# Optimization experiments

Hardware: AMD Instinct MI355X
Metric: run time of the kernel (lower is better)

The kernel has to match this reference:

```python
import jax, jax.numpy as jnp
import numpy as np

LN_EPS = 1e-5

def layer_norm(x, g, b):
    mu = jnp.mean(x, axis=-1, keepdims=True)
    var = jnp.var(x, axis=-1, keepdims=True)
    return (x - mu) * jax.lax.rsqrt(var + LN_EPS) * g + b

def setup_inputs() -> dict:
    key = jax.random.key(0)
    ks = jax.random.split(key, 4)
    d = 2048
    bs, win_len, obj_num = 8, 64, 36
    return {
        "visual_feats": jax.random.normal(ks[0], (bs, win_len, d), dtype=jnp.float32),
        "obj_feats": jax.random.normal(ks[1], (bs, win_len, obj_num, d), dtype=jnp.float32),
        "W_v": jax.random.normal(ks[2], (d, d), dtype=jnp.float32) * (1.0 / np.sqrt(d)),
        "b_v": jnp.zeros((d,), dtype=jnp.float32),
        "W_o": jax.random.normal(ks[3], (d, d), dtype=jnp.float32) * (1.0 / np.sqrt(d)),
        "b_o": jnp.zeros((d,), dtype=jnp.float32),
        "ln_v_g": jnp.ones((d,), dtype=jnp.float32),
        "ln_v_b": jnp.zeros((d,), dtype=jnp.float32),
        "ln_o_g": jnp.ones((d,), dtype=jnp.float32),
        "ln_o_b": jnp.zeros((d,), dtype=jnp.float32),
        "ln_ov_g": jnp.ones((d,), dtype=jnp.float32),
        "ln_ov_b": jnp.zeros((d,), dtype=jnp.float32),
    }

def reference(visual_feats, obj_feats, W_v, b_v, W_o, b_o,
              ln_v_g, ln_v_b, ln_o_g, ln_o_b, ln_ov_g, ln_ov_b):
    bs, win_len, obj_num, obj_size = obj_feats.shape
    # visual branch: linear -> tanh -> LN   [bs, F, d]
    ve = layer_norm(jnp.tanh(visual_feats @ W_v + b_v), ln_v_g, ln_v_b)
    # object branch: linear -> flatten frames*objects -> tanh -> LN  [bs, N, d]
    oe = (obj_feats @ W_o + b_o).reshape(bs, win_len * obj_num, obj_size)
    oe = layer_norm(jnp.tanh(oe), ln_o_g, ln_o_b)
    # adjacency: [bs, N, F], softmax over N (object axis, dim=1)
    adj = jnp.einsum('bnd,bfd->bnf', oe, ve) / jnp.sqrt(jnp.asarray(obj_size, dtype=oe.dtype))
    adj = jax.nn.softmax(adj, axis=1)
    # aggregate objects per frame: (oe^T @ adj)^T -> [bs, F, d]
    obj_agg = jnp.einsum('bnd,bnf->bfd', oe, adj)
    return layer_norm(jnp.tanh(obj_agg + ve), ln_ov_g, ln_ov_b)
```

## Files before the change

### kernel.cpp

```cpp
#include <hip/hip_runtime.h>
#include <cstdint>
#include <cstddef>


typedef __attribute__((ext_vector_type(4))) float f32x4;
typedef __attribute__((ext_vector_type(4))) unsigned int u32x4;
typedef __attribute__((ext_vector_type(8))) short bf16x8;

#define DD 2048
#define BS 8
#define FF 64
#define NOBJ 2304
#define MO 18432
#define MV 512

__device__ __forceinline__ unsigned short f2bf(float f) {
  unsigned int u = __float_as_uint(f);
  u += 0x7fffu + ((u >> 16) & 1u);
  return (unsigned short)(u >> 16);
}
__device__ __forceinline__ unsigned int pk2(float a, float b) {
  return (unsigned int)f2bf(a) | ((unsigned int)f2bf(b) << 16);
}
__device__ __forceinline__ float bf2f(unsigned short u) {
  return __uint_as_float((unsigned int)u << 16);
}

typedef __attribute__((address_space(1))) const unsigned int gas_u32;
typedef __attribute__((address_space(3))) unsigned int las_u32;
__device__ __forceinline__ void gl_lds16(const void* g, void* l) {
  __builtin_amdgcn_global_load_lds((gas_u32*)g, (las_u32*)l, 16, 0, 0);
}

__global__ __launch_bounds__(256) void k_cvt_bf16(const float* __restrict__ X,
                                                  unsigned short* __restrict__ O,
                                                  int n16) {
  int idx = blockIdx.x * 256 + threadIdx.x;
  const int stride = gridDim.x * 256;
  for (int i = idx; i < n16; i += stride) {
    const f32x4* src = (const f32x4*)(X + (size_t)i * 16);
    f32x4 a = src[0], b = src[1], c = src[2], d = src[3];
    u32x4 p = {pk2(a.x, a.y), pk2(a.z, a.w), pk2(b.x, b.y), pk2(b.z, b.w)};
    u32x4 q = {pk2(c.x, c.y), pk2(c.z, c.w), pk2(d.x, d.y), pk2(d.z, d.w)};
    u32x4* dst = (u32x4*)(O + (size_t)i * 16);
    dst[0] = p;
    dst[1] = q;
  }
}

__global__ __launch_bounds__(256) void k_wprep2(const float* __restrict__ Wv,
                                                const float* __restrict__ Wo,
                                                unsigned short* __restrict__ WvT,
                                                unsigned short* __restrict__ WoT) {
  __shared__ unsigned short sh[64][65];
  const float* W = blockIdx.z ? Wo : Wv;
  unsigned short* Wt = blockIdx.z ? WoT : WvT;
  const int t = threadIdx.x;
  const int kb = blockIdx.x * 64, nb = blockIdx.y * 64;
  {
    const int rk = t >> 2, seg = t & 3;
    const float* src = W + (size_t)(kb + rk) * DD + nb + seg * 16;
#pragma unroll
    for (int q = 0; q < 4; ++q) {
      f32x4 x = *(const f32x4*)(src + q * 4);
      sh[rk][seg * 16 + q * 4 + 0] = f2bf(x.x);
      sh[rk][seg * 16 + q * 4 + 1] = f2bf(x.y);
      sh[rk][seg * 16 + q * 4 + 2] = f2bf(x.z);
      sh[rk][seg * 16 + q * 4 + 3] = f2bf(x.w);
    }
  }
  __syncthreads();
  {
    const int nn = t >> 2, ks = t & 3;
    unsigned int o[8];
#pragma unroll
    for (int j = 0; j < 8; ++j)
      o[j] = (unsigned int)sh[ks * 16 + 2 * j][nn] |
             ((unsigned int)sh[ks * 16 + 2 * j + 1][nn] << 16);
    u32x4 p0 = {o[0], o[1], o[2], o[3]};
    u32x4 p1 = {o[4], o[5], o[6], o[7]};
    unsigned short* dst = Wt + (size_t)(nb + nn) * DD + kb + ks * 16;
    ((u32x4*)dst)[0] = p0;
    ((u32x4*)dst)[1] = p1;
  }
}

__global__ __launch_bounds__(512, 1) void k_gemm_bbf(const unsigned short* __restrict__ A,
                                                     const unsigned short* __restrict__ Bt,
                                                     const float* __restrict__ bias,
                                                     unsigned short* __restrict__ T,
                                                     float* __restrict__ part) {
  __shared__ __align__(16) unsigned short lds[2 * 32768];
  const int tid = threadIdx.x;
  const int lane = tid & 63, wave = tid >> 6;
  const int r = lane & 15, g = lane >> 4;
  const int wm = wave >> 2, wn = wave & 3;

  const int orig = blockIdx.y * 8 + blockIdx.x;
  const int lin = (orig & 7) * 72 + (orig >> 3);
  const int bm = (lin >> 3) * 256;
  const int bn = (lin & 7) * 256;

  const int srow = tid >> 3;
  const int k16s = (tid & 7) ^ (srow & 7);
  const unsigned short* aS = A + (size_t)(bm + srow) * DD + k16s * 8;
  const unsigned short* bS = Bt + (size_t)(bn + srow) * DD + k16s * 8;

  auto stage = [&](int buf, int kt) {
    unsigned short* ab = lds + buf * 32768;
    unsigned short* bb = ab + 16384;
    const size_t ko = (size_t)kt * 64;
#pragma unroll
    for (int i = 0; i < 4; ++i)
      gl_lds16(aS + ko + (size_t)(i * 64) * DD, ab + ((i * 512 + tid) << 3));
#pragma unroll
    for (int i = 0; i < 4; ++i)
      gl_lds16(bS + ko + (size_t)(i * 64) * DD, bb + ((i * 512 + tid) << 3));
  };

  const int rs = r & 7;
  const int s0 = ((0 + g) ^ rs) * 8;
  const int s1 = ((4 + g) ^ rs) * 8;
  const int abase = (wm * 128 + r) * 64;
  const int bbase = 16384 + (wn * 64 + r) * 64;

  f32x4 acc[8][4] = {};

  stage(0, 0);
  asm volatile("s_waitcnt vmcnt(0)" ::: "memory");
  __builtin_amdgcn_s_barrier();

  for (int kt = 0; kt < DD / 64; ++kt) {
    const unsigned short* bufp = lds + (kt & 1) * 32768;
    const bool st = (kt + 1 < DD / 64);
    if (st) stage((kt + 1) & 1, kt + 1);

    bf16x8 bAll[4][2];
#pragma unroll
    for (int ni = 0; ni < 4; ++ni) {
      const int ro = bbase + ni * 1024;
      bAll[ni][0] = *(const bf16x8*)(bufp + ro + s0);
      bAll[ni][1] = *(const bf16x8*)(bufp + ro + s1);
    }
#pragma unroll
    for (int q = 0; q < 4; ++q) {
      bf16x8 af[2][2];
#pragma unroll
      for (int mi = 0; mi < 2; ++mi) {
        const int ro = abase + (q * 32 + mi * 16) * 64;
        af[mi][0] = *(const bf16x8*)(bufp + ro + s0);
        af[mi][1] = *(const bf16x8*)(bufp + ro + s1);
      }
      __builtin_amdgcn_s_setprio(1);
#pragma unroll
      for (int mi = 0; mi < 2; ++mi)
#pragma unroll
        for (int ni = 0; ni < 4; ++ni) {
          acc[q * 2 + mi][ni] = __builtin_amdgcn_mfma_f32_16x16x32_bf16(
              af[mi][0], bAll[ni][0], acc[q * 2 + mi][ni], 0, 0, 0);
          acc[q * 2 + mi][ni] = __builtin_amdgcn_mfma_f32_16x16x32_bf16(
              af[mi][1], bAll[ni][1], acc[q * 2 + mi][ni], 0, 0, 0);
        }
      __builtin_amdgcn_s_setprio(0);
    }
    if (st) asm volatile("s_waitcnt vmcnt(0)" ::: "memory");
    __builtin_amdgcn_s_barrier();
  }

  float bv[4];
#pragma unroll
  for (int ni = 0; ni < 4; ++ni) bv[ni] = bias[bn + wn * 64 + ni * 16 + r];
  const int slot = ((lin & 7) << 2) + wn;
#pragma unroll
  for (int mi = 0; mi < 8; ++mi) {
#pragma unroll
    for (int i2 = 0; i2 < 4; ++i2) {
      const int row = bm + wm * 128 + mi * 16 + g * 4 + i2;
      unsigned short* trow = T + (size_t)row * DD + bn + wn * 64 + r;
      float s1 = 0.f, s2 = 0.f;
#pragma unroll
      for (int ni = 0; ni < 4; ++ni) {
        const float tv = tanhf(acc[mi][ni][i2] + bv[ni]);
        trow[ni * 16] = f2bf(tv);
        s1 += tv;
        s2 += tv * tv;
      }
#pragma unroll
      for (int m = 1; m < 16; m <<= 1) {
        s1 += __shfl_xor(s1, m, 64);
        s2 += __shfl_xor(s2, m, 64);
      }
      if (r == 0) {
        float2 p2 = make_float2(s1, s2);
        *(float2*)(part + (size_t)row * 64 + slot * 2) = p2;
      }
    }
  }
}

__global__ __launch_bounds__(256) void k_ep_ln2(const unsigned short* __restrict__ T,
                                                const float* __restrict__ part,
                                                const float* __restrict__ gw,
                                                const float* __restrict__ bw,
                                                unsigned short* __restrict__ obf) {
  const int row = blockIdx.x, t = threadIdx.x;
  float s1 = 0.f, s2 = 0.f;
  if (t < 32) {
    float2 p = ((const float2*)(part + (size_t)row * 64))[t];
    s1 = p.x;
    s2 = p.y;
  }
#pragma unroll
  for (int m = 1; m < 64; m <<= 1) {
    s1 += __shfl_xor(s1, m, 64);
    s2 += __shfl_xor(s2, m, 64);
  }
  __shared__ float sh[2];
  if (t == 0) {
    sh[0] = s1;
    sh[1] = s2;
  }
  __syncthreads();
  const float mean = sh[0] * (1.0f / DD);
  const float var = sh[1] * (1.0f / DD) - mean * mean;
  const float rstd = rsqrtf(var + 1e-5f);
  const size_t base = (size_t)row * DD + t * 8;
  u32x4 tin = *(const u32x4*)(T + base);
  f32x4 g0 = ((const f32x4*)(gw + t * 8))[0], g1 = ((const f32x4*)(gw + t * 8))[1];
  f32x4 bb0 = ((const f32x4*)(bw + t * 8))[0], bb1 = ((const f32x4*)(bw + t * 8))[1];
  float gv[8], bvv[8];
  gv[0] = g0.x; gv[1] = g0.y; gv[2] = g0.z; gv[3] = g0.w;
  gv[4] = g1.x; gv[5] = g1.y; gv[6] = g1.z; gv[7] = g1.w;
  bvv[0] = bb0.x; bvv[1] = bb0.y; bvv[2] = bb0.z; bvv[3] = bb0.w;
  bvv[4] = bb1.x; bvv[5] = bb1.y; bvv[6] = bb1.z; bvv[7] = bb1.w;
  float o[8];
#pragma unroll
  for (int j = 0; j < 4; ++j) {
    const float tl = bf2f((unsigned short)(tin[j] & 0xffffu));
    const float th = bf2f((unsigned short)(tin[j] >> 16));
    o[2 * j] = (tl - mean) * rstd * gv[2 * j] + bvv[2 * j];
    o[2 * j + 1] = (th - mean) * rstd * gv[2 * j + 1] + bvv[2 * j + 1];
  }
  u32x4 p = {pk2(o[0], o[1]), pk2(o[2], o[3]), pk2(o[4], o[5]), pk2(o[6], o[7])};
  *((u32x4*)(obf + base)) = p;
}

__global__ __launch_bounds__(256) void k_gemm_xw(const float* __restrict__ X,
                                                 const unsigned short* __restrict__ Wt,
                                                 const float* __restrict__ bias,
                                                 float* __restrict__ Y) {
  __shared__ __align__(16) unsigned short As[128 * 32];
  __shared__ __align__(16) unsigned short Bs[128 * 32];
  const int t = threadIdx.x;
  const int lane = t & 63, wave = t >> 6;
  const int r = lane & 15, g = lane >> 4;
  const int wm = wave >> 1, wn = wave & 1;
  const int bm = blockIdx.y * 128, bn = blockIdx.x * 128;
  const int arow = t >> 1, ah = t & 1;
  f32x4 acc[4][4] = {};
  const float* aptr = X + (size_t)(bm + arow) * DD + ah * 16;
  const unsigned short* bptr = Wt + (size_t)(bn + arow) * DD + ah * 16;
  for (int kt = 0; kt < DD / 32; ++kt) {
    const int kb = kt * 32;
    f32x4 a0 = *(const f32x4*)(aptr + kb);
    f32x4 a1 = *(const f32x4*)(aptr + kb + 4);
    f32x4 a2 = *(const f32x4*)(aptr + kb + 8);
    f32x4 a3 = *(const f32x4*)(aptr + kb + 12);
    u32x4 b0 = *(const u32x4*)(bptr + kb);
    u32x4 b1 = *(const u32x4*)(bptr + kb + 8);
    __syncthreads();
    u32x4 p0 = {pk2(a0.x, a0.y), pk2(a0.z, a0.w), pk2(a1.x, a1.y), pk2(a1.z, a1.w)};
    u32x4 p1 = {pk2(a2.x, a2.y), pk2(a2.z, a2.w), pk2(a3.x, a3.y), pk2(a3.z, a3.w)};
    ((u32x4*)As)[arow * 4 + ah * 2 + 0] = p0;
    ((u32x4*)As)[arow * 4 + ah * 2 + 1] = p1;
    ((u32x4*)Bs)[arow * 4 + ah * 2 + 0] = b0;
    ((u32x4*)Bs)[arow * 4 + ah * 2 + 1] = b1;
    __syncthreads();
    bf16x8 af[4], bfr[4];
#pragma unroll
    for (int m = 0; m < 4; ++m) af[m] = ((const bf16x8*)As)[(wm * 64 + m * 16 + r) * 4 + g];
#pragma unroll
    for (int n = 0; n < 4; ++n) bfr[n] = ((const bf16x8*)Bs)[(wn * 64 + n * 16 + r) * 4 + g];
#pragma unroll
    for (int m = 0; m < 4; ++m)
#pragma unroll
      for (int n = 0; n < 4; ++n)
        acc[m][n] = __builtin_amdgcn_mfma_f32_16x16x32_bf16(af[m], bfr[n], acc[m][n], 0, 0, 0);
  }
#pragma unroll
  for (int m = 0; m < 4; ++m) {
    const int row0 = bm + wm * 64 + m * 16 + g * 4;
#pragma unroll
    for (int n = 0; n < 4; ++n) {
      const int col = bn + wn * 64 + n * 16 + r;
      const float bvx = bias[col];
#pragma unroll
      for (int i = 0; i < 4; ++i)
        Y[(size_t)(row0 + i) * DD + col] = acc[m][n][i] + bvx;
    }
  }
}

__global__ __launch_bounds__(256) void k_ep_ln(const float* __restrict__ Y,
                                               const float* __restrict__ Y2,
                                               const float* __restrict__ gw,
                                               const float* __restrict__ bw,
                                               unsigned short* __restrict__ obf,
                                               float* __restrict__ of32) {
  const int row = blockIdx.x, t = threadIdx.x;
  const size_t base = (size_t)row * DD + t * 8;
  f32x4 v0 = ((const f32x4*)(Y + base))[0];
  f32x4 v1 = ((const f32x4*)(Y + base))[1];
  if (Y2 != nullptr) {
    v0 += ((const f32x4*)(Y2 + base))[0];
    v1 += ((const f32x4*)(Y2 + base))[1];
  }
  float tv[8];
#pragma unroll
  for (int j = 0; j < 4; ++j) {
    tv[j] = tanhf(v0[j]);
    tv[4 + j] = tanhf(v1[j]);
  }
  float s1 = 0.f, s2 = 0.f;
#pragma unroll
  for (int j = 0; j < 8; ++j) {
    s1 += tv[j];
    s2 += tv[j] * tv[j];
  }
#pragma unroll
  for (int m = 1; m < 64; m <<= 1) {
    s1 += __shfl_xor(s1, m, 64);
    s2 += __shfl_xor(s2, m, 64);
  }
  __shared__ float r1[4], r2[4];
  const int wave = t >> 6;
  if ((t & 63) == 0) {
    r1[wave] = s1;
    r2[wave] = s2;
  }
  __syncthreads();
  const float S1 = r1[0] + r1[1] + r1[2] + r1[3];
  const float S2 = r2[0] + r2[1] + r2[2] + r2[3];
  const float mean = S1 * (1.0f / DD);
  const float var = S2 * (1.0f / DD) - mean * mean;
  const float rstd = rsqrtf(var + 1e-5f);
  f32x4 g0 = ((const f32x4*)(gw + t * 8))[0], g1 = ((const f32x4*)(gw + t * 8))[1];
  f32x4 bb0 = ((const f32x4*)(bw + t * 8))[0], bb1 = ((const f32x4*)(bw + t * 8))[1];
  float o[8];
#pragma unroll
  for (int j = 0; j < 4; ++j) {
    o[j] = (tv[j] - mean) * rstd * g0[j] + bb0[j];
    o[4 + j] = (tv[4 + j] - mean) * rstd * g1[j] + bb1[j];
  }
  if (obf != nullptr) {
    u32x4 p = {pk2(o[0], o[1]), pk2(o[2], o[3]), pk2(o[4], o[5]), pk2(o[6], o[7])};
    *((u32x4*)(obf + base)) = p;
  }
  if (of32 != nullptr) {
    f32x4 w0 = {o[0], o[1], o[2], o[3]}, w1 = {o[4], o[5], o[6], o[7]};
    ((f32x4*)(of32 + base))[0] = w0;
    ((f32x4*)(of32 + base))[1] = w1;
  }
}

__global__ __launch_bounds__(256) void k_troe(const unsigned short* __restrict__ oe,
                                              unsigned short* __restrict__ oeT) {
  __shared__ unsigned short sh[64][65];
  const int t = threadIdx.x;
  const int b = blockIdx.z, nt = blockIdx.x, dt = blockIdx.y;
  {
    const int nn = t >> 2, seg = t & 3;
    const unsigned short* src = oe + ((size_t)b * NOBJ + nt * 64 + nn) * DD + dt * 64 + seg * 16;
    u32x4 x0 = ((const u32x4*)src)[0];
    u32x4 x1 = ((const u32x4*)src)[1];
    const unsigned short* px0 = (const unsigned short*)&x0;
    const unsigned short* px1 = (const unsigned short*)&x1;
#pragma unroll
    for (int j = 0; j < 8; ++j) {
      sh[nn][seg * 16 + j] = px0[j];
      sh[nn][seg * 16 + 8 + j] = px1[j];
    }
  }
  __syncthreads();
  {
    const int dd = t >> 2, ns = t & 3;
    unsigned int o[8];
#pragma unroll
    for (int j = 0; j < 8; ++j)
      o[j] = (unsigned int)sh[ns * 16 + 2 * j][dd] |
             ((unsigned int)sh[ns * 16 + 2 * j + 1][dd] << 16);
    u32x4 p0 = {o[0], o[1], o[2], o[3]};
    u32x4 p1 = {o[4], o[5], o[6], o[7]};
    unsigned short* dst = oeT + ((size_t)b * DD + dt * 64 + dd) * NOBJ + nt * 64 + ns * 16;
    ((u32x4*)dst)[0] = p0;
    ((u32x4*)dst)[1] = p1;
  }
}

__global__ __launch_bounds__(256) void k_gemm_adj(const unsigned short* __restrict__ oe,
                                                  const unsigned short* __restrict__ veb,
                                                  float* __restrict__ adjT) {
  __shared__ __align__(16) unsigned short As[128 * 32];
  __shared__ __align__(16) unsigned short Bs[64 * 32];
  const int t = threadIdx.x;
  const int lane = t & 63, wave = t >> 6;
  const int r = lane & 15, g = lane >> 4;
  const int wm = wave >> 1, wn = wave & 1;
  const int b = blockIdx.y, bm = blockIdx.x * 128;
  const int arow = t >> 1, ah = t & 1;
  const int br_ = t >> 2, bseg = t & 3;
  f32x4 acc[4][2] = {};
  const unsigned short* aptr = oe + ((size_t)b * NOBJ + bm + arow) * DD + ah * 16;
  const unsigned short* bptr = veb + ((size_t)b * FF + br_) * DD + bseg * 8;
  for (int kt = 0; kt < DD / 32; ++kt) {
    const int kb = kt * 32;
    u32x4 a0 = ((const u32x4*)(aptr + kb))[0];
    u32x4 a1 = ((const u32x4*)(aptr + kb))[1];
    u32x4 bvx = *(const u32x4*)(bptr + kb);
    __syncthreads();
    ((u32x4*)As)[arow * 4 + ah * 2 + 0] = a0;
    ((u32x4*)As)[arow * 4 + ah * 2 + 1] = a1;
    ((u32x4*)Bs)[br_ * 4 + bseg] = bvx;
    __syncthreads();
    bf16x8 af[4], bfr[2];
#pragma unroll
    for (int m = 0; m < 4; ++m) af[m] = ((const bf16x8*)As)[(wm * 64 + m * 16 + r) * 4 + g];
#pragma unroll
    for (int n = 0; n < 2; ++n) bfr[n] = ((const bf16x8*)Bs)[(wn * 32 + n * 16 + r) * 4 + g];
#pragma unroll
    for (int m = 0; m < 4; ++m)
#pragma unroll
      for (int n = 0; n < 2; ++n)
        acc[m][n] = __builtin_amdgcn_mfma_f32_16x16x32_bf16(af[m], bfr[n], acc[m][n], 0, 0, 0);
  }
  const float scale = 0.02209708691207961f;
#pragma unroll
  for (int m = 0; m < 4; ++m)
#pragma unroll
    for (int n = 0; n < 2; ++n) {
      const int f = wn * 32 + n * 16 + r;
      const int n0 = bm + wm * 64 + m * 16 + g * 4;
      f32x4 v = acc[m][n];
      v *= scale;
      *(f32x4*)(adjT + ((size_t)b * FF + f) * NOBJ + n0) = v;
    }
}

__global__ __launch_bounds__(256) void k_smax(const float* __restrict__ adjT,
                                              unsigned short* __restrict__ out) {
  const int t = threadIdx.x;
  const size_t base = (size_t)blockIdx.x * NOBJ;
  float v[9];
#pragma unroll
  for (int j = 0; j < 9; ++j) v[j] = adjT[base + t + j * 256];
  float m = v[0];
#pragma unroll
  for (int j = 1; j < 9; ++j) m = fmaxf(m, v[j]);
#pragma unroll
  for (int s = 1; s < 64; s <<= 1) m = fmaxf(m, __shfl_xor(m, s, 64));
  __shared__ float rm[4], rs[4];
  const int wave = t >> 6;
  if ((t & 63) == 0) rm[wave] = m;
  __syncthreads();
  m = fmaxf(fmaxf(rm[0], rm[1]), fmaxf(rm[2], rm[3]));
  float e[9];
  float s = 0.f;
#pragma unroll
  for (int j = 0; j < 9; ++j) {
    e[j] = __expf(v[j] - m);
    s += e[j];
  }
#pragma unroll
  for (int q = 1; q < 64; q <<= 1) s += __shfl_xor(s, q, 64);
  if ((t & 63) == 0) rs[wave] = s;
  __syncthreads();
  const float S = rs[0] + rs[1] + rs[2] + rs[3];
  const float inv = 1.0f / S;
#pragma unroll
  for (int j = 0; j < 9; ++j) out[base + t + j * 256] = f2bf(e[j] * inv);
}

__global__ __launch_bounds__(256) void k_gemm_agg(const unsigned short* __restrict__ adjsm,
                                                  const unsigned short* __restrict__ oeT,
                                                  float* __restrict__ agg) {
  __shared__ __align__(16) unsigned short As[64 * 32];
  __shared__ __align__(16) unsigned short Bs[128 * 32];
  const int t = threadIdx.x;
  const int lane = t & 63, wave = t >> 6;
  const int r = lane & 15, g = lane >> 4;
  const int wm = wave >> 1, wn = wave & 1;
  const int b = blockIdx.y, bn = blockIdx.x * 128;
  const int ar = t >> 2, aseg = t & 3;
  const int brow = t >> 1, bh = t & 1;
  f32x4 acc[2][4] = {};
  const unsigned short* aptr = adjsm + ((size_t)b * FF + ar) * NOBJ + aseg * 8;
  const unsigned short* bptr = oeT + ((size_t)b * DD + bn + brow) * NOBJ + bh * 16;
  for (int kt = 0; kt < NOBJ / 32; ++kt) {
    const int kb = kt * 32;
    u32x4 av = *(const u32x4*)(aptr + kb);
    u32x4 b0 = ((const u32x4*)(bptr + kb))[0];
    u32x4 b1 = ((const u32x4*)(bptr + kb))[1];
    __syncthreads();
    ((u32x4*)As)[ar * 4 + aseg] = av;
    ((u32x4*)Bs)[brow * 4 + bh * 2 + 0] = b0;
    ((u32x4*)Bs)[brow * 4 + bh * 2 + 1] = b1;
    __syncthreads();
    bf16x8 af[2], bfr[4];
#pragma unroll
    for (int m = 0; m < 2; ++m) af[m] = ((const bf16x8*)As)[(wm * 32 + m * 16 + r) * 4 + g];
#pragma unroll
    for (int n = 0; n < 4; ++n) bfr[n] = ((const bf16x8*)Bs)[(wn * 64 + n * 16 + r) * 4 + g];
#pragma unroll
    for (int m = 0; m < 2; ++m)
#pragma unroll
      for (int n = 0; n < 4; ++n)
        acc[m][n] = __builtin_amdgcn_mfma_f32_16x16x32_bf16(af[m], bfr[n], acc[m][n], 0, 0, 0);
  }
#pragma unroll
  for (int m = 0; m < 2; ++m)
#pragma unroll
    for (int n = 0; n < 4; ++n) {
      const int d = bn + wn * 64 + n * 16 + r;
#pragma unroll
      for (int i = 0; i < 4; ++i) {
        const int f = wm * 32 + m * 16 + g * 4 + i;
        agg[((size_t)b * FF + f) * DD + d] = acc[m][n][i];
      }
    }
}


extern "C" void kernel_launch(void* const* d_in, const int* in_sizes, int n_in,
                              void* d_out, int out_size, void* d_ws, size_t ws_size,
                              hipStream_t stream) {
  (void)in_sizes; (void)n_in; (void)out_size;
  const float* visual = (const float*)d_in[0];
  const float* obj    = (const float*)d_in[1];
  const float* W_v    = (const float*)d_in[2];
  const float* b_v    = (const float*)d_in[3];
  const float* W_o    = (const float*)d_in[4];
  const float* b_o    = (const float*)d_in[5];
  const float* ln_v_g = (const float*)d_in[6];
  const float* ln_v_b = (const float*)d_in[7];
  const float* ln_o_g = (const float*)d_in[8];
  const float* ln_o_b = (const float*)d_in[9];
  const float* ln_ov_g = (const float*)d_in[10];
  const float* ln_ov_b = (const float*)d_in[11];

  char* ws = (char*)d_ws;
  constexpr size_t OFF_WVT = 0;
  constexpr size_t OFF_WOT = 8ull << 20;
  constexpr size_t OFF_OBJB = 16ull << 20;
  constexpr size_t OFF_T   = 88ull << 20;
  constexpr size_t OFF_PART = 160ull << 20;
  constexpr size_t OFF_YV  = 232ull << 20;
  constexpr size_t OFF_VEF = 236ull << 20;
  constexpr size_t OFF_VEB = 240ull << 20;
  constexpr size_t OFF_ADJ = 242ull << 20;
  constexpr size_t OFF_ADJS = OFF_ADJ + 4718592ull;
  constexpr size_t OFF_AGG = OFF_ADJS + 2359296ull;
  constexpr size_t WS_NEED = OFF_AGG + 4194304ull;
  if (ws_size < WS_NEED) return;

  unsigned short* WvT  = (unsigned short*)(ws + OFF_WVT);
  unsigned short* WoT  = (unsigned short*)(ws + OFF_WOT);
  unsigned short* objb = (unsigned short*)(ws + OFF_OBJB);
  unsigned short* oe_b = (unsigned short*)(ws + OFF_OBJB);
  unsigned short* T    = (unsigned short*)(ws + OFF_T);
  unsigned short* oeT  = (unsigned short*)(ws + OFF_T);
  float* part          = (float*)(ws + OFF_PART);
  float* Yv            = (float*)(ws + OFF_YV);
  float* ve_f          = (float*)(ws + OFF_VEF);
  unsigned short* ve_b = (unsigned short*)(ws + OFF_VEB);
  float* adjT          = (float*)(ws + OFF_ADJ);
  unsigned short* adjs = (unsigned short*)(ws + OFF_ADJS);
  float* agg           = (float*)(ws + OFF_AGG);

  dim3 b256(256);
  k_wprep2<<<dim3(32, 32, 2), b256, 0, stream>>>(W_v, W_o, WvT, WoT);
  k_cvt_bf16<<<dim3(2048), b256, 0, stream>>>(obj, objb, MO * DD / 16);
  k_gemm_xw<<<dim3(16, MV / 128), b256, 0, stream>>>(visual, WvT, b_v, Yv);
  k_gemm_bbf<<<dim3(8, MO / 256), dim3(512), 0, stream>>>(objb, WoT, b_o, T, part);
  k_ep_ln<<<dim3(MV), b256, 0, stream>>>(Yv, nullptr, ln_v_g, ln_v_b, ve_b, ve_f);
  k_ep_ln2<<<dim3(MO), b256, 0, stream>>>(T, part, ln_o_g, ln_o_b, oe_b);
  k_troe<<<dim3(36, 32, 8), b256, 0, stream>>>(oe_b, oeT);
  k_gemm_adj<<<dim3(NOBJ / 128, BS), b256, 0, stream>>>(oe_b, ve_b, adjT);
  k_smax<<<dim3(MV), b256, 0, stream>>>(adjT, adjs);
  k_gemm_agg<<<dim3(DD / 128, BS), b256, 0, stream>>>(adjs, oeT, agg);
  k_ep_ln<<<dim3(MV), b256, 0, stream>>>(agg, ve_f, ln_ov_g, ln_ov_b, nullptr, (float*)d_out);
}
```

Before: 487.3 us.

## Split GEMM K-step into four barrier-separated MFMA phases with staged global loads

Restructures the main GEMM k-loop into four quadrant phases (A-top/B-left, A-top/B-right, A-bottom/B-left, A-bottom/B-right). Each phase is separated by workgroup barriers, and the A and B global-to-LDS prefetches are interleaved between phases. The aim is a ping-pong style schedule in which waves alternate LDS reads, memory issue and MFMA bursts, to better overlap memory and compute. It adds several extra barriers per k-step and changes register pressure, since A fragments for half the tile and all B fragments are held at once.

```diff
diff --git a/kernel.cpp b/kernel.cpp
--- a/kernel.cpp
+++ b/kernel.cpp
@@ -106,13 +106,16 @@
   const unsigned short* aS = A + (size_t)(bm + srow) * DD + k16s * 8;
   const unsigned short* bS = Bt + (size_t)(bn + srow) * DD + k16s * 8;
 
-  auto stage = [&](int buf, int kt) {
+  auto stageA = [&](int buf, int kt) {
     unsigned short* ab = lds + buf * 32768;
-    unsigned short* bb = ab + 16384;
     const size_t ko = (size_t)kt * 64;
 #pragma unroll
     for (int i = 0; i < 4; ++i)
       gl_lds16(aS + ko + (size_t)(i * 64) * DD, ab + ((i * 512 + tid) << 3));
+  };
+  auto stageB = [&](int buf, int kt) {
+    unsigned short* bb = lds + buf * 32768 + 16384;
+    const size_t ko = (size_t)kt * 64;
 #pragma unroll
     for (int i = 0; i < 4; ++i)
       gl_lds16(bS + ko + (size_t)(i * 64) * DD, bb + ((i * 512 + tid) << 3));
@@ -125,44 +128,89 @@
   const int bbase = 16384 + (wn * 64 + r) * 64;
 
   f32x4 acc[8][4] = {};
-
-  stage(0, 0);
+  bf16x8 aH[4][2];
+  bf16x8 bAll[4][2];
+
+  stageA(0, 0);
+  stageB(0, 0);
   asm volatile("s_waitcnt vmcnt(0)" ::: "memory");
   __builtin_amdgcn_s_barrier();
 
   for (int kt = 0; kt < DD / 64; ++kt) {
     const unsigned short* bufp = lds + (kt & 1) * 32768;
     const bool st = (kt + 1 < DD / 64);
-    if (st) stage((kt + 1) & 1, kt + 1);
-
-    bf16x8 bAll[4][2];
-#pragma unroll
-    for (int ni = 0; ni < 4; ++ni) {
+
+#pragma unroll
+    for (int mi = 0; mi < 4; ++mi) {
+      const int ro = abase + mi * 1024;
+      aH[mi][0] = *(const bf16x8*)(bufp + ro + s0);
+      aH[mi][1] = *(const bf16x8*)(bufp + ro + s1);
+    }
+#pragma unroll
+    for (int ni = 0; ni < 2; ++ni) {
       const int ro = bbase + ni * 1024;
       bAll[ni][0] = *(const bf16x8*)(bufp + ro + s0);
       bAll[ni][1] = *(const bf16x8*)(bufp + ro + s1);
     }
-#pragma unroll
-    for (int q = 0; q < 4; ++q) {
-      bf16x8 af[2][2];
-#pragma unroll
-      for (int mi = 0; mi < 2; ++mi) {
-        const int ro = abase + (q * 32 + mi * 16) * 64;
-        af[mi][0] = *(const bf16x8*)(bufp + ro + s0);
-        af[mi][1] = *(const bf16x8*)(bufp + ro + s1);
-      }
-      __builtin_amdgcn_s_setprio(1);
-#pragma unroll
-      for (int mi = 0; mi < 2; ++mi)
-#pragma unroll
-        for (int ni = 0; ni < 4; ++ni) {
-          acc[q * 2 + mi][ni] = __builtin_amdgcn_mfma_f32_16x16x32_bf16(
-              af[mi][0], bAll[ni][0], acc[q * 2 + mi][ni], 0, 0, 0);
-          acc[q * 2 + mi][ni] = __builtin_amdgcn_mfma_f32_16x16x32_bf16(
-              af[mi][1], bAll[ni][1], acc[q * 2 + mi][ni], 0, 0, 0);
-        }
-      __builtin_amdgcn_s_setprio(0);
-    }
+    if (st) stageA((kt + 1) & 1, kt + 1);
+    __builtin_amdgcn_s_barrier();
+    __builtin_amdgcn_s_setprio(1);
+#pragma unroll
+    for (int mi = 0; mi < 4; ++mi)
+#pragma unroll
+      for (int ni = 0; ni < 2; ++ni) {
+        acc[mi][ni] = __builtin_amdgcn_mfma_f32_16x16x32_bf16(aH[mi][0], bAll[ni][0], acc[mi][ni], 0, 0, 0);
+        acc[mi][ni] = __builtin_amdgcn_mfma_f32_16x16x32_bf16(aH[mi][1], bAll[ni][1], acc[mi][ni], 0, 0, 0);
+      }
+    __builtin_amdgcn_s_setprio(0);
+    __builtin_amdgcn_s_barrier();
+
+#pragma unroll
+    for (int ni = 2; ni < 4; ++ni) {
+      const int ro = bbase + ni * 1024;
+      bAll[ni][0] = *(const bf16x8*)(bufp + ro + s0);
+      bAll[ni][1] = *(const bf16x8*)(bufp + ro + s1);
+    }
+    if (st) stageB((kt + 1) & 1, kt + 1);
+    __builtin_amdgcn_s_barrier();
+    __builtin_amdgcn_s_setprio(1);
+#pragma unroll
+    for (int mi = 0; mi < 4; ++mi)
+#pragma unroll
+      for (int ni = 2; ni < 4; ++ni) {
+        acc[mi][ni] = __builtin_amdgcn_mfma_f32_16x16x32_bf16(aH[mi][0], bAll[ni][0], acc[mi][ni], 0, 0, 0);
+        acc[mi][ni] = __builtin_amdgcn_mfma_f32_16x16x32_bf16(aH[mi][1], bAll[ni][1], acc[mi][ni], 0, 0, 0);
+      }
+    __builtin_amdgcn_s_setprio(0);
+    __builtin_amdgcn_s_barrier();
+
+#pragma unroll
+    for (int mi = 0; mi < 4; ++mi) {
+      const int ro = abase + (64 + mi * 16) * 64;
+      aH[mi][0] = *(const bf16x8*)(bufp + ro + s0);
+      aH[mi][1] = *(const bf16x8*)(bufp + ro + s1);
+    }
+    __builtin_amdgcn_s_barrier();
+    __builtin_amdgcn_s_setprio(1);
+#pragma unroll
+    for (int mi = 0; mi < 4; ++mi)
+#pragma unroll
+      for (int ni = 0; ni < 2; ++ni) {
+        acc[4 + mi][ni] = __builtin_amdgcn_mfma_f32_16x16x32_bf16(aH[mi][0], bAll[ni][0], acc[4 + mi][ni], 0, 0, 0);
+        acc[4 + mi][ni] = __builtin_amdgcn_mfma_f32_16x16x32_bf16(aH[mi][1], bAll[ni][1], acc[4 + mi][ni], 0, 0, 0);
+      }
+    __builtin_amdgcn_s_setprio(0);
+    __builtin_amdgcn_s_barrier();
+
+    __builtin_amdgcn_s_setprio(1);
+#pragma unroll
+    for (int mi = 0; mi < 4; ++mi)
+#pragma unroll
+      for (int ni = 2; ni < 4; ++ni) {
+        acc[4 + mi][ni] = __builtin_amdgcn_mfma_f32_16x16x32_bf16(aH[mi][0], bAll[ni][0], acc[4 + mi][ni], 0, 0, 0);
+        acc[4 + mi][ni] = __builtin_amdgcn_mfma_f32_16x16x32_bf16(aH[mi][1], bAll[ni][1], acc[4 + mi][ni], 0, 0, 0);
+      }
+    __builtin_amdgcn_s_setprio(0);
     if (st) asm volatile("s_waitcnt vmcnt(0)" ::: "memory");
     __builtin_amdgcn_s_barrier();
   }
```

Measured after the change: 486.8 us. About the same (-0.1%).

## Triple-buffer big GEMM with 256x128 tiles; shrink adj/agg GEMM tiles

Applied to the files above, without the earlier changes.

The main object-projection GEMM moves from 256x256 tiles with double buffering to 256x128 tiles with a three-stage LDS pipeline. It keeps two stages in flight and waits with vmcnt(6) instead of draining all loads every iteration. The adjacency and aggregation GEMMs halve their tile width to 64, doubling the grid to raise occupancy across CUs. In exchange, each output tile does less reuse, so more global traffic is needed for the same work, and the LN partial-sum slot layout changes to 32 slots per row.

```diff
diff --git a/kernel.cpp b/kernel.cpp
--- a/kernel.cpp
+++ b/kernel.cpp
@@ -90,92 +90,96 @@
                                                      const float* __restrict__ bias,
                                                      unsigned short* __restrict__ T,
                                                      float* __restrict__ part) {
-  __shared__ __align__(16) unsigned short lds[2 * 32768];
+  __shared__ __align__(16) unsigned short lds[3 * 24576];
   const int tid = threadIdx.x;
   const int lane = tid & 63, wave = tid >> 6;
   const int r = lane & 15, g = lane >> 4;
-  const int wm = wave >> 2, wn = wave & 3;
-
-  const int orig = blockIdx.y * 8 + blockIdx.x;
-  const int lin = (orig & 7) * 72 + (orig >> 3);
-  const int bm = (lin >> 3) * 256;
-  const int bn = (lin & 7) * 256;
+  const int wm = wave >> 1, wn = wave & 1;
+
+  const int orig = blockIdx.y * 16 + blockIdx.x;
+  const int lin = (orig & 7) * 144 + (orig >> 3);
+  const int bm = (lin >> 4) * 256;
+  const int bn = (lin & 15) * 128;
 
   const int srow = tid >> 3;
   const int k16s = (tid & 7) ^ (srow & 7);
-  const unsigned short* aS = A + (size_t)(bm + srow) * DD + k16s * 8;
-  const unsigned short* bS = Bt + (size_t)(bn + srow) * DD + k16s * 8;
+  const unsigned short* aSrc[4];
+#pragma unroll
+  for (int q = 0; q < 4; ++q)
+    aSrc[q] = A + (size_t)(bm + q * 64 + srow) * DD + k16s * 8;
+  const unsigned short* bSrc[2];
+#pragma unroll
+  for (int q = 0; q < 2; ++q)
+    bSrc[q] = Bt + (size_t)(bn + q * 64 + srow) * DD + k16s * 8;
 
   auto stage = [&](int buf, int kt) {
-    unsigned short* ab = lds + buf * 32768;
+    unsigned short* ab = lds + buf * 24576;
     unsigned short* bb = ab + 16384;
     const size_t ko = (size_t)kt * 64;
 #pragma unroll
-    for (int i = 0; i < 4; ++i)
-      gl_lds16(aS + ko + (size_t)(i * 64) * DD, ab + ((i * 512 + tid) << 3));
-#pragma unroll
-    for (int i = 0; i < 4; ++i)
-      gl_lds16(bS + ko + (size_t)(i * 64) * DD, bb + ((i * 512 + tid) << 3));
+    for (int q = 0; q < 4; ++q)
+      gl_lds16(aSrc[q] + ko, ab + ((q * 512 + tid) << 3));
+#pragma unroll
+    for (int q = 0; q < 2; ++q)
+      gl_lds16(bSrc[q] + ko, bb + ((q * 512 + tid) << 3));
   };
 
   const int rs = r & 7;
-  const int s0 = ((0 + g) ^ rs) * 8;
-  const int s1 = ((4 + g) ^ rs) * 8;
-  const int abase = (wm * 128 + r) * 64;
-  const int bbase = 16384 + (wn * 64 + r) * 64;
-
-  f32x4 acc[8][4] = {};
-
+  const int sa0 = ((0 + g) ^ rs) * 8;
+  const int sa1 = ((4 + g) ^ rs) * 8;
+  const int arow0 = wm * 64 + r;
+  const int brow0 = wn * 64 + r;
+
+  f32x4 acc[4][4] = {};
   stage(0, 0);
-  asm volatile("s_waitcnt vmcnt(0)" ::: "memory");
+  stage(1, 1);
+  asm volatile("s_waitcnt vmcnt(6)" ::: "memory");
   __builtin_amdgcn_s_barrier();
 
   for (int kt = 0; kt < DD / 64; ++kt) {
-    const unsigned short* bufp = lds + (kt & 1) * 32768;
-    const bool st = (kt + 1 < DD / 64);
-    if (st) stage((kt + 1) & 1, kt + 1);
-
-    bf16x8 bAll[4][2];
+    const int cur = kt % 3;
+    if (kt + 2 < DD / 64) stage((kt + 2) % 3, kt + 2);
+    const unsigned short* ab = lds + cur * 24576;
+    const unsigned short* bb = ab + 16384;
+    bf16x8 af[4][2], bfr[4][2];
+#pragma unroll
+    for (int mi = 0; mi < 4; ++mi) {
+      const int ro = (arow0 + mi * 16) * 64;
+      af[mi][0] = *(const bf16x8*)(ab + ro + sa0);
+      af[mi][1] = *(const bf16x8*)(ab + ro + sa1);
+    }
 #pragma unroll
     for (int ni = 0; ni < 4; ++ni) {
-      const int ro = bbase + ni * 1024;
-      bAll[ni][0] = *(const bf16x8*)(bufp + ro + s0);
-      bAll[ni][1] = *(const bf16x8*)(bufp + ro + s1);
-    }
-#pragma unroll
-    for (int q = 0; q < 4; ++q) {
-      bf16x8 af[2][2];
-#pragma unroll
-      for (int mi = 0; mi < 2; ++mi) {
-        const int ro = abase + (q * 32 + mi * 16) * 64;
-        af[mi][0] = *(const bf16x8*)(bufp + ro + s0);
-        af[mi][1] = *(const bf16x8*)(bufp + ro + s1);
+      const int ro = (brow0 + ni * 16) * 64;
+      bfr[ni][0] = *(const bf16x8*)(bb + ro + sa0);
+      bfr[ni][1] = *(const bf16x8*)(bb + ro + sa1);
+    }
+    __builtin_amdgcn_s_setprio(1);
+#pragma unroll
+    for (int mi = 0; mi < 4; ++mi)
+#pragma unroll
+      for (int ni = 0; ni < 4; ++ni) {
+        acc[mi][ni] = __builtin_amdgcn_mfma_f32_16x16x32_bf16(af[mi][0], bfr[ni][0], acc[mi][ni], 0, 0, 0);
+        acc[mi][ni] = __builtin_amdgcn_mfma_f32_16x16x32_bf16(af[mi][1], bfr[ni][1], acc[mi][ni], 0, 0, 0);
       }
-      __builtin_amdgcn_s_setprio(1);
-#pragma unroll
-      for (int mi = 0; mi < 2; ++mi)
-#pragma unroll
-        for (int ni = 0; ni < 4; ++ni) {
-          acc[q * 2 + mi][ni] = __builtin_amdgcn_mfma_f32_16x16x32_bf16(
-              af[mi][0], bAll[ni][0], acc[q * 2 + mi][ni], 0, 0, 0);
-          acc[q * 2 + mi][ni] = __builtin_amdgcn_mfma_f32_16x16x32_bf16(
-              af[mi][1], bAll[ni][1], acc[q * 2 + mi][ni], 0, 0, 0);
-        }
-      __builtin_amdgcn_s_setprio(0);
-    }
-    if (st) asm volatile("s_waitcnt vmcnt(0)" ::: "memory");
+    __builtin_amdgcn_s_setprio(0);
+    if (kt < DD / 64 - 2) {
+      asm volatile("s_waitcnt vmcnt(6)" ::: "memory");
+    } else {
+      asm volatile("s_waitcnt vmcnt(0)" ::: "memory");
+    }
     __builtin_amdgcn_s_barrier();
   }
 
   float bv[4];
 #pragma unroll
   for (int ni = 0; ni < 4; ++ni) bv[ni] = bias[bn + wn * 64 + ni * 16 + r];
-  const int slot = ((lin & 7) << 2) + wn;
-#pragma unroll
-  for (int mi = 0; mi < 8; ++mi) {
+  const int slot = ((lin & 15) << 1) + wn;
+#pragma unroll
+  for (int mi = 0; mi < 4; ++mi) {
 #pragma unroll
     for (int i2 = 0; i2 < 4; ++i2) {
-      const int row = bm + wm * 128 + mi * 16 + g * 4 + i2;
+      const int row = bm + wm * 64 + mi * 16 + g * 4 + i2;
       unsigned short* trow = T + (size_t)row * DD + bn + wn * 64 + r;
       float s1 = 0.f, s2 = 0.f;
 #pragma unroll
@@ -400,46 +404,43 @@
 __global__ __launch_bounds__(256) void k_gemm_adj(const unsigned short* __restrict__ oe,
                                                   const unsigned short* __restrict__ veb,
                                                   float* __restrict__ adjT) {
-  __shared__ __align__(16) unsigned short As[128 * 32];
+  __shared__ __align__(16) unsigned short As[64 * 32];
   __shared__ __align__(16) unsigned short Bs[64 * 32];
   const int t = threadIdx.x;
   const int lane = t & 63, wave = t >> 6;
   const int r = lane & 15, g = lane >> 4;
   const int wm = wave >> 1, wn = wave & 1;
-  const int b = blockIdx.y, bm = blockIdx.x * 128;
-  const int arow = t >> 1, ah = t & 1;
-  const int br_ = t >> 2, bseg = t & 3;
-  f32x4 acc[4][2] = {};
-  const unsigned short* aptr = oe + ((size_t)b * NOBJ + bm + arow) * DD + ah * 16;
-  const unsigned short* bptr = veb + ((size_t)b * FF + br_) * DD + bseg * 8;
+  const int b = blockIdx.y, bm = blockIdx.x * 64;
+  const int arow = t >> 2, aseg = t & 3;
+  f32x4 acc[2][2] = {};
+  const unsigned short* aptr = oe + ((size_t)b * NOBJ + bm + arow) * DD + aseg * 8;
+  const unsigned short* bptr = veb + ((size_t)b * FF + arow) * DD + aseg * 8;
   for (int kt = 0; kt < DD / 32; ++kt) {
     const int kb = kt * 32;
-    u32x4 a0 = ((const u32x4*)(aptr + kb))[0];
-    u32x4 a1 = ((const u32x4*)(aptr + kb))[1];
+    u32x4 a0 = *(const u32x4*)(aptr + kb);
     u32x4 bvx = *(const u32x4*)(bptr + kb);
     __syncthreads();
-    ((u32x4*)As)[arow * 4 + ah * 2 + 0] = a0;
-    ((u32x4*)As)[arow * 4 + ah * 2 + 1] = a1;
-    ((u32x4*)Bs)[br_ * 4 + bseg] = bvx;
+    ((u32x4*)As)[arow * 4 + aseg] = a0;
+    ((u32x4*)Bs)[arow * 4 + aseg] = bvx;
     __syncthreads();
-    bf16x8 af[4], bfr[2];
-#pragma unroll
-    for (int m = 0; m < 4; ++m) af[m] = ((const bf16x8*)As)[(wm * 64 + m * 16 + r) * 4 + g];
+    bf16x8 af[2], bfr[2];
+#pragma unroll
+    for (int m = 0; m < 2; ++m) af[m] = ((const bf16x8*)As)[(wm * 32 + m * 16 + r) * 4 + g];
 #pragma unroll
     for (int n = 0; n < 2; ++n) bfr[n] = ((const bf16x8*)Bs)[(wn * 32 + n * 16 + r) * 4 + g];
 #pragma unroll
-    for (int m = 0; m < 4; ++m)
+    for (int m = 0; m < 2; ++m)
 #pragma unroll
       for (int n = 0; n < 2; ++n)
         acc[m][n] = __builtin_amdgcn_mfma_f32_16x16x32_bf16(af[m], bfr[n], acc[m][n], 0, 0, 0);
   }
   const float scale = 0.02209708691207961f;
 #pragma unroll
-  for (int m = 0; m < 4; ++m)
+  for (int m = 0; m < 2; ++m)
 #pragma unroll
     for (int n = 0; n < 2; ++n) {
       const int f = wn * 32 + n * 16 + r;
-      const int n0 = bm + wm * 64 + m * 16 + g * 4;
+      const int n0 = bm + wm * 32 + m * 16 + g * 4;
       f32x4 v = acc[m][n];
       v *= scale;
       *(f32x4*)(adjT + ((size_t)b * FF + f) * NOBJ + n0) = v;
@@ -484,43 +485,40 @@
                                                   const unsigned short* __restrict__ oeT,
                                                   float* __restrict__ agg) {
   __shared__ __align__(16) unsigned short As[64 * 32];
-  __shared__ __align__(16) unsigned short Bs[128 * 32];
+  __shared__ __align__(16) unsigned short Bs[64 * 32];
   const int t = threadIdx.x;
   const int lane = t & 63, wave = t >> 6;
   const int r = lane & 15, g = lane >> 4;
   const int wm = wave >> 1, wn = wave & 1;
-  const int b = blockIdx.y, bn = blockIdx.x * 128;
-  const int ar = t >> 2, aseg = t & 3;
-  const int brow = t >> 1, bh = t & 1;
-  f32x4 acc[2][4] = {};
-  const unsigned short* aptr = adjsm + ((size_t)b * FF + ar) * NOBJ + aseg * 8;
-  const unsigned short* bptr = oeT + ((size_t)b * DD + bn + brow) * NOBJ + bh * 16;
+  const int b = blockIdx.y, bn = blockIdx.x * 64;
+  const int arow = t >> 2, aseg = t & 3;
+  f32x4 acc[2][2] = {};
+  const unsigned short* aptr = adjsm + ((size_t)b * FF + arow) * NOBJ + aseg * 8;
+  const unsigned short* bptr = oeT + ((size_t)b * DD + bn + arow) * NOBJ + aseg * 8;
   for (int kt = 0; kt < NOBJ / 32; ++kt) {
     const int kb = kt * 32;
     u32x4 av = *(const u32x4*)(aptr + kb);
-    u32x4 b0 = ((const u32x4*)(bptr + kb))[0];
-    u32x4 b1 = ((const u32x4*)(bptr + kb))[1];
+    u32x4 bvx = *(const u32x4*)(bptr + kb);
     __syncthreads();
-    ((u32x4*)As)[ar * 4 + aseg] = av;
-    ((u32x4*)Bs)[brow * 4 + bh * 2 + 0] = b0;
-    ((u32x4*)Bs)[brow * 4 + bh * 2 + 1] = b1;
+    ((u32x4*)As)[arow * 4 + aseg] = av;
+    ((u32x4*)Bs)[arow * 4 + aseg] = bvx;
     __syncthreads();
-    bf16x8 af[2], bfr[4];
+    bf16x8 af[2], bfr[2];
 #pragma unroll
     for (int m = 0; m < 2; ++m) af[m] = ((const bf16x8*)As)[(wm * 32 + m * 16 + r) * 4 + g];
 #pragma unroll
-    for (int n = 0; n < 4; ++n) bfr[n] = ((const bf16x8*)Bs)[(wn * 64 + n * 16 + r) * 4 + g];
+    for (int n = 0; n < 2; ++n) bfr[n] = ((const bf16x8*)Bs)[(wn * 32 + n * 16 + r) * 4 + g];
 #pragma unroll
     for (int m = 0; m < 2; ++m)
 #pragma unroll
-      for (int n = 0; n < 4; ++n)
+      for (int n = 0; n < 2; ++n)
         acc[m][n] = __builtin_amdgcn_mfma_f32_16x16x32_bf16(af[m], bfr[n], acc[m][n], 0, 0, 0);
   }
 #pragma unroll
   for (int m = 0; m < 2; ++m)
 #pragma unroll
-    for (int n = 0; n < 4; ++n) {
-      const int d = bn + wn * 64 + n * 16 + r;
+    for (int n = 0; n < 2; ++n) {
+      const int d = bn + wn * 32 + n * 16 + r;
 #pragma unroll
       for (int i = 0; i < 4; ++i) {
         const int f = wm * 32 + m * 16 + g * 4 + i;
@@ -580,12 +578,12 @@
   k_wprep2<<<dim3(32, 32, 2), b256, 0, stream>>>(W_v, W_o, WvT, WoT);
   k_cvt_bf16<<<dim3(2048), b256, 0, stream>>>(obj, objb, MO * DD / 16);
   k_gemm_xw<<<dim3(16, MV / 128), b256, 0, stream>>>(visual, WvT, b_v, Yv);
-  k_gemm_bbf<<<dim3(8, MO / 256), dim3(512), 0, stream>>>(objb, WoT, b_o, T, part);
+  k_gemm_bbf<<<dim3(16, MO / 256), dim3(512), 0, stream>>>(objb, WoT, b_o, T, part);
   k_ep_ln<<<dim3(MV), b256, 0, stream>>>(Yv, nullptr, ln_v_g, ln_v_b, ve_b, ve_f);
   k_ep_ln2<<<dim3(MO), b256, 0, stream>>>(T, part, ln_o_g, ln_o_b, oe_b);
   k_troe<<<dim3(36, 32, 8), b256, 0, stream>>>(oe_b, oeT);
-  k_gemm_adj<<<dim3(NOBJ / 128, BS), b256, 0, stream>>>(oe_b, ve_b, adjT);
+  k_gemm_adj<<<dim3(NOBJ / 64, BS), b256, 0, stream>>>(oe_b, ve_b, adjT);
   k_smax<<<dim3(MV), b256, 0, stream>>>(adjT, adjs);
-  k_gemm_agg<<<dim3(DD / 128, BS), b256, 0, stream>>>(adjs, oeT, agg);
+  k_gemm_agg<<<dim3(DD / 64, BS), b256, 0, stream>>>(adjs, oeT, agg);
   k_ep_ln<<<dim3(MV), b256, 0, stream>>>(agg, ve_f, ln_ov_g, ln_ov_b, nullptr, (float*)d_out);
 }
```

After: 457.6 us. 6.1% less time.
